# Kernel optimization log

Measured on AMD Instinct MI355X. Metric: run time of the kernel, lower is better.

Reference implementation:

```python
import jax, jax.numpy as jnp
import numpy as np

B, H, L, C = 16, 512, 4096, 1
LAM = 0.001  # kernel squash threshold (lam in LongConvKernel)


def setup_inputs() -> dict:
    key = jax.random.key(0)
    ks = jax.random.split(key, 5)
    u = jax.random.normal(ks[0], (B, H, L), jnp.float32)
    # LongConvKernel 'double_exp' init: K ~ N(0, 0.02^2) * exp(-(j/L) * (H//2)^(i/H))
    K = jax.random.normal(ks[1], (C, H, L), jnp.float32) * 0.02
    i = jnp.arange(H, dtype=jnp.float32)[:, None]
    j = jnp.arange(L, dtype=jnp.float32)[None, :]
    double_exp = jnp.exp(-(j / L) * jnp.power(float(H // 2), i / H))  # (H, L)
    kernel = K * double_exp[None]
    D = jax.random.normal(ks[2], (C, H), jnp.float32)  # skip connection params
    # TransposedLinear(C*H -> H): weight (d_output, d_input), kaiming-ish scale
    Wout = jax.random.normal(ks[3], (H, C * H), jnp.float32) / np.sqrt(C * H)
    bout = jax.random.normal(ks[4], (H,), jnp.float32) * 0.01
    return {"u": u, "kernel": kernel, "D": D, "Wout": Wout, "bout": bout}


def reference(u, kernel, D, Wout, bout):
    Lseq = u.shape[-1]
    # kernel squashing: relu(|k| - lam) * sign(k)  (soft-threshold)
    k = jax.nn.relu(jnp.abs(kernel) - LAM) * jnp.sign(kernel)  # (C, H, L)
    n = 2 * Lseq
    k_f = jnp.fft.rfft(k, n=n, axis=-1)            # (C, H, n//2+1) complex
    u_f = jnp.fft.rfft(u, n=n, axis=-1)            # (B, H, n//2+1) complex
    y_f = jnp.einsum('bhl,chl->bchl', u_f, k_f)    # pointwise multiply in freq
    y = jnp.fft.irfft(y_f, n=n, axis=-1)[..., :Lseq]  # (B, C, H, L)
    y = y + jnp.einsum('bhl,ch->bchl', u, D)       # skip term
    y = y.reshape(y.shape[0], C * H, Lseq)         # (B, C*H, L)
    y = jax.nn.gelu(y, approximate=False)          # activation (torch GELU = exact)
    # output_linear: TransposedLinear + swish postact
    y = jnp.einsum('bul,vu->bvl', y, Wout) + bout[None, :, None]
    y = jax.nn.silu(y)
    return y
```

## Files before the change

### kernel.cpp

```cpp
#include <hip/hip_runtime.h>
#include <hip/hip_bf16.h>
#include <math.h>

#define BB 16
#define HH 512
#define LL 4096
#define NFFT 8192
#define LAM 0.001f

typedef __attribute__((ext_vector_type(8))) short short8;
typedef __attribute__((ext_vector_type(4))) float floatx4;

#define R2C 0.70710678118654752f

__device__ __forceinline__ void cmul(float ar, float ai, float br, float bi,
                                     float& cr, float& ci) {
  cr = ar * br - ai * bi;
  ci = ar * bi + ai * br;
}

constexpr float W16C[8] = {1.f, 0.92387953f, 0.70710678f, 0.38268343f, 0.f,
                           -0.38268343f, -0.70710678f, -0.92387953f};
constexpr float W16S[8] = {0.f, -0.38268343f, -0.70710678f, -0.92387953f, -1.f,
                           -0.92387953f, -0.70710678f, -0.38268343f};
constexpr int BR8[8] = {0, 4, 2, 6, 1, 5, 3, 7};
constexpr float W16CB[8] = {W16C[0], W16C[4], W16C[2], W16C[6],
                            W16C[1], W16C[5], W16C[3], W16C[7]};
constexpr float W16SB[8] = {W16S[0], W16S[4], W16S[2], W16S[6],
                            W16S[1], W16S[5], W16S[3], W16S[7]};

__device__ __forceinline__ int slotf(int a) { return a ^ ((a >> 4) & 15); }

__device__ __forceinline__ void fft8(float* r, float* i) {
  float t0r = r[0] + r[4], t0i = i[0] + i[4], u0r = r[0] - r[4], u0i = i[0] - i[4];
  float t1r = r[1] + r[5], t1i = i[1] + i[5], u1r = r[1] - r[5], u1i = i[1] - i[5];
  float t2r = r[2] + r[6], t2i = i[2] + i[6], u2r = r[2] - r[6], u2i = i[2] - i[6];
  float t3r = r[3] + r[7], t3i = i[3] + i[7], u3r = r[3] - r[7], u3i = i[3] - i[7];
  float w1r = R2C * (u1r + u1i), w1i = R2C * (u1i - u1r);
  float w2r = u2i, w2i = -u2r;
  float w3r = R2C * (u3i - u3r), w3i = -R2C * (u3r + u3i);
  float p0r = t0r + t2r, p0i = t0i + t2i, q0r = t0r - t2r, q0i = t0i - t2i;
  float p1r = t1r + t3r, p1i = t1i + t3i, q1r = t1r - t3r, q1i = t1i - t3i;
  float s1r = q1i, s1i = -q1r;
  float v0r = u0r + w2r, v0i = u0i + w2i, x0r = u0r - w2r, x0i = u0i - w2i;
  float v1r = w1r + w3r, v1i = w1i + w3i, x1r = w1r - w3r, x1i = w1i - w3i;
  float y1r = x1i, y1i = -x1r;
  r[0] = p0r + p1r; i[0] = p0i + p1i;
  r[1] = p0r - p1r; i[1] = p0i - p1i;
  r[2] = q0r + s1r; i[2] = q0i + s1i;
  r[3] = q0r - s1r; i[3] = q0i - s1i;
  r[4] = v0r + v1r; i[4] = v0i + v1i;
  r[5] = v0r - v1r; i[5] = v0i - v1i;
  r[6] = x0r + y1r; i[6] = x0i + y1i;
  r[7] = x0r - y1r; i[7] = x0i - y1i;
}

__device__ __forceinline__ void fft8_pad4(float* r, float* i) {
  float x0r = r[0], x0i = i[0], x1r = r[1], x1i = i[1];
  float x2r = r[2], x2i = i[2], x3r = r[3], x3i = i[3];
  float w1r = R2C * (x1r + x1i), w1i = R2C * (x1i - x1r);
  float w2r = x2i, w2i = -x2r;
  float w3r = R2C * (x3i - x3r), w3i = -R2C * (x3r + x3i);
  float p0r = x0r + x2r, p0i = x0i + x2i, q0r = x0r - x2r, q0i = x0i - x2i;
  float p1r = x1r + x3r, p1i = x1i + x3i, q1r = x1r - x3r, q1i = x1i - x3i;
  float s1r = q1i, s1i = -q1r;
  float v0r = x0r + w2r, v0i = x0i + w2i, m0r = x0r - w2r, m0i = x0i - w2i;
  float v1r = w1r + w3r, v1i = w1i + w3i, m1r = w1r - w3r, m1i = w1i - w3i;
  float y1r = m1i, y1i = -m1r;
  r[0] = p0r + p1r; i[0] = p0i + p1i;
  r[1] = p0r - p1r; i[1] = p0i - p1i;
  r[2] = q0r + s1r; i[2] = q0i + s1i;
  r[3] = q0r - s1r; i[3] = q0i - s1i;
  r[4] = v0r + v1r; i[4] = v0i + v1i;
  r[5] = v0r - v1r; i[5] = v0i - v1i;
  r[6] = m0r + y1r; i[6] = m0i + y1i;
  r[7] = m0r - y1r; i[7] = m0i - y1i;
}

__device__ __forceinline__ void ifft8(float* r, float* i) {
  float p0r = r[0] + r[1], p0i = i[0] + i[1];
  float p1r = r[0] - r[1], p1i = i[0] - i[1];
  float q0r = r[2] + r[3], q0i = i[2] + i[3];
  float s1r = r[2] - r[3], s1i = i[2] - i[3];
  float v0r = r[4] + r[5], v0i = i[4] + i[5];
  float v1r = r[4] - r[5], v1i = i[4] - i[5];
  float x0r = r[6] + r[7], x0i = i[6] + i[7];
  float y1r = r[6] - r[7], y1i = i[6] - i[7];
  float q1r = -s1i, q1i = s1r;
  float x1r = -y1i, x1i = y1r;
  float t0r = p0r + q0r, t0i = p0i + q0i, t2r = p0r - q0r, t2i = p0i - q0i;
  float t1r = p1r + q1r, t1i = p1i + q1i, t3r = p1r - q1r, t3i = p1i - q1i;
  float a0r = v0r + x0r, a0i = v0i + x0i, a2r = v0r - x0r, a2i = v0i - x0i;
  float a1r = v1r + x1r, a1i = v1i + x1i, a3r = v1r - x1r, a3i = v1i - x1i;
  float u1r = R2C * (a1r - a1i), u1i = R2C * (a1r + a1i);
  float u2r = -a2i, u2i = a2r;
  float u3r = -R2C * (a3r + a3i), u3i = R2C * (a3r - a3i);
  r[0] = t0r + a0r; i[0] = t0i + a0i;  r[4] = t0r - a0r; i[4] = t0i - a0i;
  r[1] = t1r + u1r; i[1] = t1i + u1i;  r[5] = t1r - u1r; i[5] = t1i - u1i;
  r[2] = t2r + u2r; i[2] = t2i + u2i;  r[6] = t2r - u2r; i[6] = t2i - u2i;
  r[3] = t3r + u3r; i[3] = t3i + u3i;  r[7] = t3r - u3r; i[7] = t3i - u3i;
}

__device__ __forceinline__ void ifft8_head4(float* r, float* i) {
  float p0r = r[0] + r[1], p0i = i[0] + i[1];
  float p1r = r[0] - r[1], p1i = i[0] - i[1];
  float q0r = r[2] + r[3], q0i = i[2] + i[3];
  float s1r = r[2] - r[3], s1i = i[2] - i[3];
  float v0r = r[4] + r[5], v0i = i[4] + i[5];
  float v1r = r[4] - r[5], v1i = i[4] - i[5];
  float x0r = r[6] + r[7], x0i = i[6] + i[7];
  float y1r = r[6] - r[7], y1i = i[6] - i[7];
  float q1r = -s1i, q1i = s1r;
  float x1r = -y1i, x1i = y1r;
  float t0r = p0r + q0r, t0i = p0i + q0i, t2r = p0r - q0r, t2i = p0i - q0i;
  float t1r = p1r + q1r, t1i = p1i + q1i, t3r = p1r - q1r, t3i = p1i - q1i;
  float a0r = v0r + x0r, a0i = v0i + x0i, a2r = v0r - x0r, a2i = v0i - x0i;
  float a1r = v1r + x1r, a1i = v1i + x1i, a3r = v1r - x1r, a3i = v1i - x1i;
  float u1r = R2C * (a1r - a1i), u1i = R2C * (a1r + a1i);
  float u2r = -a2i, u2i = a2r;
  float u3r = -R2C * (a3r + a3i), u3i = R2C * (a3r - a3i);
  r[0] = t0r + a0r; i[0] = t0i + a0i;
  r[1] = t1r + u1r; i[1] = t1i + u1i;
  r[2] = t2r + u2r; i[2] = t2i + u2i;
  r[3] = t3r + u3r; i[3] = t3i + u3i;
}

__device__ __forceinline__ float gelu_exact(float y) {
  return 0.5f * y * (1.f + erff(y * 0.70710678118654752f));
}

template <int LOGJ>
__device__ __forceinline__ void r8_fwd(float2* sb, int t, const float4* tw) {
  const int J = 1 << LOGJ;
  const int j = t & (J - 1);
  const int base = (t >> LOGJ) << (LOGJ + 3);
  float xr[8], xi[8];
#pragma unroll
  for (int s = 0; s < 8; ++s) {
    float2 v = sb[slotf(base + j + (s << LOGJ))];
    xr[s] = v.x; xi[s] = v.y;
  }
  fft8(xr, xi);
#pragma unroll
  for (int q = 0; q < 4; ++q) {
    float4 w = tw[(q << LOGJ) + j];
    float tr, ti;
    cmul(xr[2 * q], xi[2 * q], w.x, w.y, tr, ti);
    sb[slotf(base + (BR8[2 * q] << LOGJ) + j)] = make_float2(tr, ti);
    cmul(xr[2 * q + 1], xi[2 * q + 1], w.z, w.w, tr, ti);
    sb[slotf(base + (BR8[2 * q + 1] << LOGJ) + j)] = make_float2(tr, ti);
  }
}

template <int LOGJ>
__device__ __forceinline__ void r8_inv(float2* sb, int t, const float4* tw) {
  const int J = 1 << LOGJ;
  const int j = t & (J - 1);
  const int base = (t >> LOGJ) << (LOGJ + 3);
  float xr[8], xi[8];
#pragma unroll
  for (int q = 0; q < 4; ++q) {
    float4 w = tw[(q << LOGJ) + j];
    float2 v0 = sb[slotf(base + (BR8[2 * q] << LOGJ) + j)];
    cmul(v0.x, v0.y, w.x, -w.y, xr[2 * q], xi[2 * q]);
    float2 v1 = sb[slotf(base + (BR8[2 * q + 1] << LOGJ) + j)];
    cmul(v1.x, v1.y, w.z, -w.w, xr[2 * q + 1], xi[2 * q + 1]);
  }
  ifft8(xr, xi);
#pragma unroll
  for (int s = 0; s < 8; ++s)
    sb[slotf(base + j + (s << LOGJ))] = make_float2(xr[s], xi[s]);
}

__device__ __forceinline__ void p1_scatter(float2* sb, int j, const float4* tw1,
                                           float* xr, float* xi) {
#pragma unroll
  for (int q = 0; q < 4; ++q) {
    float4 w = tw1[(q << 10) + j];
    float tr, ti;
    cmul(xr[2 * q], xi[2 * q], w.x, w.y, tr, ti);
    sb[slotf((BR8[2 * q] << 10) + j)] = make_float2(tr, ti);
    cmul(xr[2 * q + 1], xi[2 * q + 1], w.z, w.w, tr, ti);
    sb[slotf((BR8[2 * q + 1] << 10) + j)] = make_float2(tr, ti);
  }
}

__device__ __forceinline__ void p4_bins(float2* sb, int t, float* br_, float* bi_) {
  const int p = t >> 1, par = t & 1;
  const int a0 = (p << 4) + par;
  float xr[8], xi[8];
#pragma unroll
  for (int e = 0; e < 8; ++e) {
    float2 v = sb[slotf(a0 + 2 * e)];
    xr[e] = v.x; xi[e] = v.y;
  }
  fft8(xr, xi);
#pragma unroll
  for (int s = 0; s < 8; ++s) {
    float tr, ti;
    if (par) { cmul(xr[s], xi[s], W16CB[s], W16SB[s], tr, ti); }
    else { tr = xr[s]; ti = xi[s]; }
    float orr = __shfl_xor(tr, 1);
    float oii = __shfl_xor(ti, 1);
    br_[s] = par ? (orr - tr) : (tr + orr);
    bi_[s] = par ? (oii - ti) : (ti + oii);
  }
}

__device__ __forceinline__ void p4_inv(float2* sb, int t, float* br_, float* bi_) {
  const int p = t >> 1, par = t & 1;
  const int a0 = (p << 4) + par;
  float yr[8], yi[8];
#pragma unroll
  for (int s = 0; s < 8; ++s) {
    float orr = __shfl_xor(br_[s], 1);
    float oii = __shfl_xor(bi_[s], 1);
    float er = par ? (orr - br_[s]) : (br_[s] + orr);
    float ei = par ? (oii - bi_[s]) : (bi_[s] + oii);
    if (par) { float tr, ti; cmul(er, ei, W16CB[s], -W16SB[s], tr, ti); er = tr; ei = ti; }
    yr[s] = er; yi[s] = ei;
  }
  ifft8(yr, yi);
#pragma unroll
  for (int e = 0; e < 8; ++e)
    sb[slotf(a0 + 2 * e)] = make_float2(yr[e], yi[e]);
}

__global__ __launch_bounds__(1024) void twgen_kernel(float4* __restrict__ tw1,
                                                     float4* __restrict__ tw2,
                                                     float4* __restrict__ tw3) {
  const int j = threadIdx.x;
#pragma unroll
  for (int q = 0; q < 4; ++q) {
    const int m0 = BR8[2 * q], m1 = BR8[2 * q + 1];
    float s0, c0, s1, c1;
    const float a1 = -6.283185307179586f / 8192.f;
    sincosf(a1 * (float)(j * m0), &s0, &c0);
    sincosf(a1 * (float)(j * m1), &s1, &c1);
    tw1[(q << 10) + j] = make_float4(c0, s0, c1, s1);
    if (j < 128) {
      const float a2 = -6.283185307179586f / 1024.f;
      sincosf(a2 * (float)(j * m0), &s0, &c0);
      sincosf(a2 * (float)(j * m1), &s1, &c1);
      tw2[(q << 7) + j] = make_float4(c0, s0, c1, s1);
    }
    if (j < 16) {
      const float a3 = -6.283185307179586f / 128.f;
      sincosf(a3 * (float)(j * m0), &s0, &c0);
      sincosf(a3 * (float)(j * m1), &s1, &c1);
      tw3[(q << 4) + j] = make_float4(c0, s0, c1, s1);
    }
  }
}

__global__ void wconv_kernel(const float* __restrict__ W,
                             __hip_bfloat16* __restrict__ Wb) {
  int i = blockIdx.x * 256 + threadIdx.x;
  Wb[i] = __float2bfloat16(W[i]);
}

__global__ __launch_bounds__(1024)
void kf_kernel(const float* __restrict__ kern, const float* __restrict__ D,
               float* __restrict__ Kf, const float4* __restrict__ tw1,
               const float4* __restrict__ tw2, const float4* __restrict__ tw3) {
  __shared__ __align__(16) float2 sb[NFFT];
  __shared__ __align__(16) float4 ltw2[512];
  __shared__ __align__(16) float4 ltw3[64];
  const int t = threadIdx.x;
  const int h = blockIdx.x;
  const float* kr = kern + (size_t)h * LL;
  if (t < 512) ltw2[t] = tw2[t];
  if (t < 64) ltw3[t] = tw3[t];
  {
    float xr[8], xi[8];
#pragma unroll
    for (int s = 0; s < 4; ++s) {
      float kv = kr[t + (s << 10)];
      float a = fabsf(kv) - LAM;
      float sq = (a > 0.f) ? ((kv > 0.f) ? a : -a) : 0.f;
      xr[s] = sq * (1.f / 8192.f);
      xi[s] = 0.f;
    }
    fft8_pad4(xr, xi);
    p1_scatter(sb, t, tw1, xr, xi);
  }
  __syncthreads();
  r8_fwd<7>(sb, t, ltw2);
  __syncthreads();
  r8_fwd<4>(sb, t, ltw3);
  {
    float br_[8], bi_[8];
    p4_bins(sb, t, br_, bi_);
    const float dsc = D[h] * (1.f / 8192.f);
    float4* out4 = (float4*)(Kf + (size_t)h * NFFT * 2) + (t << 2);
#pragma unroll
    for (int q = 0; q < 4; ++q)
      out4[q] = make_float4(br_[2 * q] + dsc, bi_[2 * q],
                            br_[2 * q + 1] + dsc, bi_[2 * q + 1]);
  }
}

__global__ __launch_bounds__(1024)
void fftconv_kernel(const float* __restrict__ u, const float* __restrict__ Kf,
                    __hip_bfloat16* __restrict__ g, const float4* __restrict__ tw1,
                    const float4* __restrict__ tw2, const float4* __restrict__ tw3) {
  __shared__ __align__(16) float2 sb[NFFT];
  __shared__ __align__(16) float4 ltw2[512];
  __shared__ __align__(16) float4 ltw3[64];
  const int t = threadIdx.x;
  const int h = blockIdx.x;
  const int p = blockIdx.y;
  const int b0 = 2 * p, b1 = 2 * p + 1;
  const float* u0 = u + ((size_t)(b0 * HH + h)) * LL;
  const float* u1 = u + ((size_t)(b1 * HH + h)) * LL;

  if (t < 512) ltw2[t] = tw2[t];
  if (t < 64) ltw3[t] = tw3[t];

  {
    float xr[8], xi[8];
#pragma unroll
    for (int s = 0; s < 4; ++s) {
      xr[s] = u0[t + (s << 10)];
      xi[s] = u1[t + (s << 10)];
    }
    fft8_pad4(xr, xi);
    p1_scatter(sb, t, tw1, xr, xi);
  }
  __syncthreads();
  r8_fwd<7>(sb, t, ltw2);
  __syncthreads();
  r8_fwd<4>(sb, t, ltw3);
  {
    float br_[8], bi_[8];
    p4_bins(sb, t, br_, bi_);
    const float4* kf4 = (const float4*)(Kf + (size_t)h * NFFT * 2) + (t << 2);
#pragma unroll
    for (int q = 0; q < 4; ++q) {
      float4 kk = kf4[q];
      float tr, ti;
      cmul(br_[2 * q], bi_[2 * q], kk.x, kk.y, tr, ti);
      br_[2 * q] = tr; bi_[2 * q] = ti;
      cmul(br_[2 * q + 1], bi_[2 * q + 1], kk.z, kk.w, tr, ti);
      br_[2 * q + 1] = tr; bi_[2 * q + 1] = ti;
    }
    p4_inv(sb, t, br_, bi_);
  }
  r8_inv<4>(sb, t, ltw3);
  __syncthreads();
  r8_inv<7>(sb, t, ltw2);
  __syncthreads();
  {
    float xr[8], xi[8];
#pragma unroll
    for (int q = 0; q < 4; ++q) {
      float4 w = tw1[(q << 10) + t];
      float2 v0 = sb[slotf((BR8[2 * q] << 10) + t)];
      cmul(v0.x, v0.y, w.x, -w.y, xr[2 * q], xi[2 * q]);
      float2 v1 = sb[slotf((BR8[2 * q + 1] << 10) + t)];
      cmul(v1.x, v1.y, w.z, -w.w, xr[2 * q + 1], xi[2 * q + 1]);
    }
    ifft8_head4(xr, xi);
    __hip_bfloat16* g0 = g + ((size_t)(b0 * HH + h)) * LL;
    __hip_bfloat16* g1 = g + ((size_t)(b1 * HH + h)) * LL;
#pragma unroll
    for (int s = 0; s < 4; ++s) {
      g0[t + (s << 10)] = __float2bfloat16(gelu_exact(xr[s]));
      g1[t + (s << 10)] = __float2bfloat16(gelu_exact(xi[s]));
    }
  }
}

#define BKP 40
__global__ __launch_bounds__(256, 4) void gemm_kernel(
    const __hip_bfloat16* __restrict__ Wb, const __hip_bfloat16* __restrict__ g,
    const float* __restrict__ bout, float* __restrict__ out) {
  __shared__ unsigned short bt[2][128][BKP];
  const int id = blockIdx.x;
  const int w = (id & 7) * 256 + (id >> 3);
  const int vt = w & 3;
  const int lt = (w >> 2) & 31;
  const int b = w >> 7;
  const int tid = threadIdx.x;
  const int wave = tid >> 6;
  const int ln = tid & 63;
  const int wr = wave >> 1, wc = wave & 1;
  const int vbase = vt * 128 + wr * 64;
  const int lbase0 = lt * 128;
  const int lane16 = ln & 15;
  const int quad = ln >> 4;

  floatx4 acc[4][4];
#pragma unroll
  for (int mi = 0; mi < 4; ++mi)
#pragma unroll
    for (int ni = 0; ni < 4; ++ni) acc[mi][ni] = (floatx4){0.f, 0.f, 0.f, 0.f};

  const unsigned short* A = (const unsigned short*)Wb;
  const unsigned short* gb = (const unsigned short*)g + (size_t)b * HH * LL;

#define STAGE_B(BUF, K0)                                                       \
  {                                                                            \
    _Pragma("unroll") for (int it = 0; it < 2; ++it) {                         \
      const int uu = tid + it * 256;                                           \
      const int ho = uu >> 4;                                                  \
      const int lo = (uu & 15) * 8;                                            \
      int4 v = *(const int4*)(gb + (size_t)((K0) + ho) * LL + lbase0 + lo);    \
      unsigned short vs[8];                                                    \
      *(int4*)vs = v;                                                          \
      _Pragma("unroll") for (int e = 0; e < 8; ++e) bt[BUF][lo + e][ho] = vs[e]; \
    }                                                                          \
  }

  STAGE_B(0, 0);
  __syncthreads();

  for (int s = 0; s < 16; ++s) {
    const int cur = s & 1;
    if (s < 15) STAGE_B(cur ^ 1, (s + 1) * 32);
    const int kk = quad * 8;
    short8 af[4], bf[4];
#pragma unroll
    for (int mi = 0; mi < 4; ++mi) {
      const int m = vbase + mi * 16 + lane16;
      af[mi] = *(const short8*)(A + (size_t)m * HH + s * 32 + kk);
    }
#pragma unroll
    for (int ni = 0; ni < 4; ++ni) {
      const int nloc = wc * 64 + ni * 16 + lane16;
      bf[ni] = *(const short8*)(&bt[cur][nloc][kk]);
    }
#pragma unroll
    for (int mi = 0; mi < 4; ++mi)
#pragma unroll
      for (int ni = 0; ni < 4; ++ni)
        acc[mi][ni] = __builtin_amdgcn_mfma_f32_16x16x32_bf16(af[mi], bf[ni],
                                                              acc[mi][ni], 0, 0, 0);
    __syncthreads();
  }

#pragma unroll
  for (int mi = 0; mi < 4; ++mi) {
#pragma unroll
    for (int r = 0; r < 4; ++r) {
      const int m = vbase + mi * 16 + quad * 4 + r;
      const float bias = bout[m];
#pragma unroll
      for (int ni = 0; ni < 4; ++ni) {
        const int n = lbase0 + wc * 64 + ni * 16 + lane16;
        float y = acc[mi][ni][r] + bias;
        y = y / (1.f + __expf(-y));
        out[((size_t)(b * HH + m)) * LL + n] = y;
      }
    }
  }
#undef STAGE_B
}

extern "C" void kernel_launch(void* const* d_in, const int* in_sizes, int n_in,
                              void* d_out, int out_size, void* d_ws, size_t ws_size,
                              hipStream_t stream) {
  const float* u = (const float*)d_in[0];
  const float* kern = (const float*)d_in[1];
  const float* D = (const float*)d_in[2];
  const float* Wout = (const float*)d_in[3];
  const float* bout = (const float*)d_in[4];
  float* out = (float*)d_out;

  char* ws = (char*)d_ws;
  const size_t KF_BYTES = (size_t)HH * NFFT * sizeof(float2);
  const size_t G_BYTES = (size_t)BB * HH * LL * 2;
  float* Kf = (float*)ws;
  __hip_bfloat16* g = (__hip_bfloat16*)(ws + KF_BYTES);
  __hip_bfloat16* Wb = (__hip_bfloat16*)(ws + KF_BYTES + 2 * G_BYTES);
  float4* tw1 = (float4*)(ws + KF_BYTES + G_BYTES);
  float4* tw2 = tw1 + 4 * 1024;
  float4* tw3 = tw2 + 4 * 128;

  twgen_kernel<<<dim3(1), dim3(1024), 0, stream>>>(tw1, tw2, tw3);
  wconv_kernel<<<dim3((HH * HH) / 256), dim3(256), 0, stream>>>(Wout, Wb);
  kf_kernel<<<dim3(HH), dim3(1024), 0, stream>>>(kern, D, Kf, tw1, tw2, tw3);
  fftconv_kernel<<<dim3(HH, BB / 2), dim3(1024), 0, stream>>>(u, Kf, g, tw1, tw2, tw3);
  gemm_kernel<<<dim3(2048), dim3(256), 0, stream>>>(Wb, g, bout, out);
}
```

Before: 531.4 us.

## Stage GEMM weight tile in LDS, swizzle B tile, and overlap global loads with MFMA

The GEMM kernel now copies the weight (A) tile into shared memory instead of having each wave read it directly from global memory. The transposed activation tile (B) uses an XOR-swizzled layout in place of padding, to cut LDS bank conflicts. Global loads for the next K-step are issued into registers before the MFMAs and written to LDS after them, so load latency is hidden behind compute. This costs extra registers and LDS, which may lower occupancy.

```diff
diff --git a/kernel.cpp b/kernel.cpp
--- a/kernel.cpp
+++ b/kernel.cpp
@@ -371,11 +371,11 @@
   }
 }
 
-#define BKP 40
 __global__ __launch_bounds__(256, 4) void gemm_kernel(
     const __hip_bfloat16* __restrict__ Wb, const __hip_bfloat16* __restrict__ g,
     const float* __restrict__ bout, float* __restrict__ out) {
-  __shared__ unsigned short bt[2][128][BKP];
+  __shared__ unsigned short At[2][128][40];
+  __shared__ unsigned short Bt[2][4096];
   const int id = blockIdx.x;
   const int w = (id & 7) * 256 + (id >> 3);
   const int vt = w & 3;
@@ -385,10 +385,17 @@
   const int wave = tid >> 6;
   const int ln = tid & 63;
   const int wr = wave >> 1, wc = wave & 1;
-  const int vbase = vt * 128 + wr * 64;
-  const int lbase0 = lt * 128;
   const int lane16 = ln & 15;
   const int quad = ln >> 4;
+  const int lbase0 = lt * 128;
+
+  const int a_m = tid >> 2;
+  const int a_c = (tid & 3) * 8;
+  const int b_h = tid >> 4;
+  const int b_l = (tid & 15) * 8;
+
+  const unsigned short* Ag = (const unsigned short*)Wb + (size_t)(vt * 128) * HH;
+  const unsigned short* gb = (const unsigned short*)g + (size_t)b * HH * LL + lbase0;
 
   floatx4 acc[4][4];
 #pragma unroll
@@ -396,39 +403,49 @@
 #pragma unroll
     for (int ni = 0; ni < 4; ++ni) acc[mi][ni] = (floatx4){0.f, 0.f, 0.f, 0.f};
 
-  const unsigned short* A = (const unsigned short*)Wb;
-  const unsigned short* gb = (const unsigned short*)g + (size_t)b * HH * LL;
-
-#define STAGE_B(BUF, K0)                                                       \
-  {                                                                            \
-    _Pragma("unroll") for (int it = 0; it < 2; ++it) {                         \
-      const int uu = tid + it * 256;                                           \
-      const int ho = uu >> 4;                                                  \
-      const int lo = (uu & 15) * 8;                                            \
-      int4 v = *(const int4*)(gb + (size_t)((K0) + ho) * LL + lbase0 + lo);    \
-      unsigned short vs[8];                                                    \
-      *(int4*)vs = v;                                                          \
-      _Pragma("unroll") for (int e = 0; e < 8; ++e) bt[BUF][lo + e][ho] = vs[e]; \
-    }                                                                          \
-  }
-
-  STAGE_B(0, 0);
-  __syncthreads();
-
+  int4 la0, la1, lb0, lb1;
+#define GLOAD(K0)                                                         \
+  la0 = *(const int4*)(Ag + (size_t)a_m * HH + (K0) + a_c);               \
+  la1 = *(const int4*)(Ag + (size_t)(a_m + 64) * HH + (K0) + a_c);        \
+  lb0 = *(const int4*)(gb + (size_t)((K0) + b_h) * LL + b_l);             \
+  lb1 = *(const int4*)(gb + (size_t)((K0) + b_h + 16) * LL + b_l);
+#define LWRITE(BUF)                                                       \
+  *(int4*)&At[BUF][a_m][a_c] = la0;                                       \
+  *(int4*)&At[BUF][a_m + 64][a_c] = la1;                                  \
+  {                                                                       \
+    unsigned short vs[8];                                                 \
+    *(int4*)vs = lb0;                                                     \
+    _Pragma("unroll") for (int e = 0; e < 8; ++e) {                       \
+      const int l = b_l + e;                                              \
+      const int blk = (l * 4 + (b_h >> 3)) ^ ((l >> 3) & 7);              \
+      Bt[BUF][blk * 8 + (b_h & 7)] = vs[e];                               \
+    }                                                                     \
+    *(int4*)vs = lb1;                                                     \
+    _Pragma("unroll") for (int e = 0; e < 8; ++e) {                       \
+      const int l = b_l + e;                                              \
+      const int h2 = b_h + 16;                                            \
+      const int blk = (l * 4 + (h2 >> 3)) ^ ((l >> 3) & 7);               \
+      Bt[BUF][blk * 8 + (h2 & 7)] = vs[e];                                \
+    }                                                                     \
+  }
+
+  GLOAD(0);
+  LWRITE(0);
+  __syncthreads();
+
+  const int kk = quad * 8;
   for (int s = 0; s < 16; ++s) {
     const int cur = s & 1;
-    if (s < 15) STAGE_B(cur ^ 1, (s + 1) * 32);
-    const int kk = quad * 8;
+    if (s < 15) { GLOAD((s + 1) * 32); }
     short8 af[4], bf[4];
 #pragma unroll
-    for (int mi = 0; mi < 4; ++mi) {
-      const int m = vbase + mi * 16 + lane16;
-      af[mi] = *(const short8*)(A + (size_t)m * HH + s * 32 + kk);
-    }
+    for (int mi = 0; mi < 4; ++mi)
+      af[mi] = *(const short8*)&At[cur][wr * 64 + mi * 16 + lane16][kk];
 #pragma unroll
     for (int ni = 0; ni < 4; ++ni) {
       const int nloc = wc * 64 + ni * 16 + lane16;
-      bf[ni] = *(const short8*)(&bt[cur][nloc][kk]);
+      const int blk = (nloc * 4 + quad) ^ ((nloc >> 3) & 7);
+      bf[ni] = *(const short8*)&Bt[cur][blk * 8];
     }
 #pragma unroll
     for (int mi = 0; mi < 4; ++mi)
@@ -436,6 +453,7 @@
       for (int ni = 0; ni < 4; ++ni)
         acc[mi][ni] = __builtin_amdgcn_mfma_f32_16x16x32_bf16(af[mi], bf[ni],
                                                               acc[mi][ni], 0, 0, 0);
+    if (s < 15) { LWRITE(cur ^ 1); }
     __syncthreads();
   }
 
@@ -443,7 +461,7 @@
   for (int mi = 0; mi < 4; ++mi) {
 #pragma unroll
     for (int r = 0; r < 4; ++r) {
-      const int m = vbase + mi * 16 + quad * 4 + r;
+      const int m = vt * 128 + wr * 64 + mi * 16 + quad * 4 + r;
       const float bias = bout[m];
 #pragma unroll
       for (int ni = 0; ni < 4; ++ni) {
@@ -454,7 +472,8 @@
       }
     }
   }
-#undef STAGE_B
+#undef GLOAD
+#undef LWRITE
 }
 
 extern "C" void kernel_launch(void* const* d_in, const int* in_sizes, int n_in,
```

After: 477.9 us. -10.1%, faster.
